# Kernel tuning notes

Measured on AMD Instinct MI355X. Metric: run time of the kernel, lower is better.

The kernel has to match this reference:

```python
import jax, jax.numpy as jnp
import numpy as np

B, S, H, D = 2, 2048, 16, 64


def setup_inputs() -> dict:
    key0 = jax.random.key(0)
    kq, kk = jax.random.split(key0)
    query = jax.random.normal(kq, (B, S, H, D), dtype=jnp.float32)
    key = jax.random.normal(kk, (B, S, H, D), dtype=jnp.float32)
    # causal mask, broadcastable to [B, H, q, k]
    mask = jnp.tril(jnp.ones((S, S), dtype=bool))[None, None, :, :]
    mask = jnp.broadcast_to(mask, (B, 1, S, S))
    return {"query": query, "key": key, "mask": mask}


def reference(query, key, mask):
    dtype = query.dtype
    qk_features = query.shape[-1]
    q = query / jnp.sqrt(qk_features).astype(dtype)
    # [B, H, q, k]
    attn_weights = jnp.einsum('...qhd,...khd->...hqk', q, key)
    big_neg = jnp.finfo(dtype).min
    attn_weights = jnp.where(mask, attn_weights, big_neg)
    attn_weights = jax.nn.softmax(attn_weights).astype(dtype)
    return attn_weights
```

## Files before the change

kernel.cpp:

```cpp
#include <hip/hip_runtime.h>
#include <stdint.h>
#include <stddef.h>

#define B_ 2
#define H_ 16
#define S_ 2048
#define D_ 64

#define TQ 32
#define TK 256
#define NW 4
#define BLK (NW*64)
#define NQT (S_/TQ)
#define NBLK_F (B_*H_*NQT)
#define NBLK_S (32*36)
#define NBLK_W (32*8*4)

typedef __attribute__((ext_vector_type(8))) short bf16x8;
typedef __attribute__((ext_vector_type(4))) float f32x4;

__device__ __forceinline__ unsigned short f2bf(float f) {
  union { float f; uint32_t u; } v; v.f = f;
  uint32_t r = v.u + 0x7FFFu + ((v.u >> 16) & 1u);
  return (unsigned short)(r >> 16);
}

__device__ __forceinline__ void stage_k(const f32x4* kp, unsigned short* ldsK,
                                        int b, int h, int kc, int tid) {
#pragma unroll
  for (int i = 0; i < 8; ++i) {
    const int g  = i * BLK + tid;
    const int kl = g >> 3;
    const int gd = g & 7;
    const size_t gb = (((size_t)b * S_ + (kc * TK + kl)) * H_ + h) * (D_ / 4) + gd * 2;
    f32x4 v0 = kp[gb];
    f32x4 v1 = kp[gb + 1];
    bf16x8 bv;
    bv[0] = (short)f2bf(v0.x); bv[1] = (short)f2bf(v0.y);
    bv[2] = (short)f2bf(v0.z); bv[3] = (short)f2bf(v0.w);
    bv[4] = (short)f2bf(v1.x); bv[5] = (short)f2bf(v1.y);
    bv[6] = (short)f2bf(v1.z); bv[7] = (short)f2bf(v1.w);
    const int idx = (kl * D_ + gd * 8) ^ ((kl & 7) << 3);
    *reinterpret_cast<bf16x8*>(&ldsK[idx]) = bv;
  }
}

__device__ __forceinline__ void stage_q(const f32x4* qp, unsigned short (*ldsQ)[72],
                                        int b, int h, int qb, int tid) {
#pragma unroll
  for (int i = 0; i < 2; ++i) {
    const int g   = i * BLK + tid;
    const int row = g >> 4;
    const int d4  = g & 15;
    f32x4 v = qp[(((size_t)b * S_ + (qb + row)) * H_ + h) * (D_ / 4) + d4];
    unsigned short* dst = &ldsQ[row][d4 * 4];
    dst[0] = f2bf(v.x * 0.125f);
    dst[1] = f2bf(v.y * 0.125f);
    dst[2] = f2bf(v.z * 0.125f);
    dst[3] = f2bf(v.w * 0.125f);
  }
}

__device__ __forceinline__ void mfma_tile(const unsigned short* ldsK,
                                          const bf16x8 qfr[2][2],
                                          f32x4 acc[4][2], int w, int colk, int rg) {
#pragma unroll
  for (int kf = 0; kf < 4; ++kf) {
    const int krow = w * 64 + kf * 16 + colk;
    const int i0 = (krow * D_ + rg * 8) ^ ((krow & 7) << 3);
    const int i1 = (krow * D_ + 32 + rg * 8) ^ ((krow & 7) << 3);
    bf16x8 a0 = *reinterpret_cast<const bf16x8*>(&ldsK[i0]);
    bf16x8 a1 = *reinterpret_cast<const bf16x8*>(&ldsK[i1]);
#pragma unroll
    for (int qf = 0; qf < 2; ++qf) {
      acc[kf][qf] = __builtin_amdgcn_mfma_f32_16x16x32_bf16(a0, qfr[qf][0], acc[kf][qf], 0, 0, 0);
      acc[kf][qf] = __builtin_amdgcn_mfma_f32_16x16x32_bf16(a1, qfr[qf][1], acc[kf][qf], 0, 0, 0);
    }
  }
}

__device__ __forceinline__ void load_qfr(const unsigned short (*ldsQ)[72],
                                         bf16x8 qfr[2][2], int colk, int rg) {
#pragma unroll
  for (int qf = 0; qf < 2; ++qf)
#pragma unroll
    for (int hh = 0; hh < 2; ++hh)
      qfr[qf][hh] = *reinterpret_cast<const bf16x8*>(&ldsQ[qf * 16 + colk][hh * 32 + rg * 8]);
}

__global__ __launch_bounds__(BLK, 4)
void attn_sums_v4(const float* __restrict__ Qg, const float* __restrict__ Kg,
                  float* __restrict__ wsPart) {
  __shared__ unsigned short ldsK[TK * D_];
  __shared__ unsigned short ldsQ[TQ][72];
  __shared__ float ldsSum[NW][2][16];

  const int tid  = threadIdx.x;
  const int lane = tid & 63;
  const int w    = tid >> 6;
  const int colk = lane & 15;
  const int rg   = lane >> 4;

  int bid = (int)blockIdx.x;
  bid = (bid & 7) * (NBLK_S / 8) + (bid >> 3);
  const int bh = bid / 36;
  int j = bid - bh * 36;
  int kc = 0, base = 0;
  while (j >= base + (8 - kc)) { base += 8 - kc; ++kc; }
  const int ci = j - base;
  const int qt0 = kc * 8 + ci * 8;
  const int b = bh >> 4, h = bh & (H_ - 1);

  const f32x4* qp = reinterpret_cast<const f32x4*>(Qg);
  const f32x4* kp = reinterpret_cast<const f32x4*>(Kg);

  stage_k(kp, ldsK, b, h, kc, tid);

  for (int i = 0; i < 8; ++i) {
    const int qt = qt0 + i;
    const int qb = qt * TQ;
    __syncthreads();
    stage_q(qp, ldsQ, b, h, qb, tid);
    __syncthreads();
    bf16x8 qfr[2][2];
    load_qfr(ldsQ, qfr, colk, rg);
    f32x4 acc[4][2];
#pragma unroll
    for (int kf = 0; kf < 4; ++kf)
#pragma unroll
      for (int qf = 0; qf < 2; ++qf) acc[kf][qf] = (f32x4)0.0f;
    mfma_tile(ldsK, qfr, acc, w, colk, rg);

    float rsum[2] = {0.f, 0.f};
#pragma unroll
    for (int kf = 0; kf < 4; ++kf)
#pragma unroll
      for (int qf = 0; qf < 2; ++qf)
#pragma unroll
        for (int r = 0; r < 4; ++r) {
          const int kk = kc * TK + w * 64 + kf * 16 + rg * 4 + r;
          const int qq = qb + qf * 16 + colk;
          rsum[qf] += (kk <= qq) ? __expf(acc[kf][qf][r]) : 0.f;
        }
#pragma unroll
    for (int qf = 0; qf < 2; ++qf) {
      float v = rsum[qf];
      v += __shfl_xor(v, 16);
      v += __shfl_xor(v, 32);
      rsum[qf] = v;
    }
    if (rg == 0) { ldsSum[w][0][colk] = rsum[0]; ldsSum[w][1][colk] = rsum[1]; }
    __syncthreads();
    if (tid < 32) {
      const int qf = tid >> 4, ck = tid & 15;
      const float s = ldsSum[0][qf][ck] + ldsSum[1][qf][ck] +
                      ldsSum[2][qf][ck] + ldsSum[3][qf][ck];
      wsPart[((size_t)bh * 8 + kc) * S_ + qb + tid] = s;
    }
  }
}

__global__ __launch_bounds__(BLK, 4)
void attn_store_v4(const float* __restrict__ Qg, const float* __restrict__ Kg,
                   const float* __restrict__ wsPart, float* __restrict__ Og) {
  __shared__ unsigned short ldsK[TK * D_];
  __shared__ unsigned short ldsQ[TQ][72];
  __shared__ float rinvL[512];

  const int tid  = threadIdx.x;
  const int lane = tid & 63;
  const int w    = tid >> 6;
  const int colk = lane & 15;
  const int rg   = lane >> 4;

  int bid = (int)blockIdx.x;
  bid = (bid & 7) * (NBLK_W / 8) + (bid >> 3);
  const int bh = bid >> 5;
  const int r5 = bid & 31;
  const int kc = r5 >> 2;
  const int qg = r5 & 3;
  const int b = bh >> 4, h = bh & (H_ - 1);
  const int kmin = kc * TK;
  const int row0 = qg * 512;

  if (kmin > row0 + 511) {
    const int rr = tid >> 3, cg = tid & 7;
    f32x4 z = {0.f, 0.f, 0.f, 0.f};
#pragma unroll
    for (int tr = 0; tr < 16; ++tr) {
      float* rp = Og + ((size_t)bh * S_ + row0 + tr * 32 + rr) * S_ + kmin;
#pragma unroll
      for (int c = 0; c < 8; ++c)
        __builtin_nontemporal_store(z, reinterpret_cast<f32x4*>(rp + (c * 8 + cg) * 4));
    }
    return;
  }

  const f32x4* qp = reinterpret_cast<const f32x4*>(Qg);
  const f32x4* kp = reinterpret_cast<const f32x4*>(Kg);

  stage_k(kp, ldsK, b, h, kc, tid);

  for (int lr = tid; lr < 512; lr += BLK) {
    const int q = row0 + lr;
    if (q >= kmin) {
      float s = 0.f;
      const int top = q >> 8;
      for (int c2 = 0; c2 <= top; ++c2)
        s += wsPart[((size_t)bh * 8 + c2) * S_ + q];
      rinvL[lr] = 1.0f / s;
    }
  }

  bool synced = false;
  for (int i = 0; i < 16; ++i) {
    const int qt = qg * 16 + i;
    const int qb = qt * TQ;
    float* outT = Og + ((size_t)bh * S_ + qb) * S_ + kmin;

    if (kmin > qb + 31) {
      const int rr = tid >> 3, cg = tid & 7;
      f32x4 z = {0.f, 0.f, 0.f, 0.f};
      float* rp = outT + (size_t)rr * S_;
#pragma unroll
      for (int c = 0; c < 8; ++c)
        __builtin_nontemporal_store(z, reinterpret_cast<f32x4*>(rp + (c * 8 + cg) * 4));
      continue;
    }

    __syncthreads();
    (void)synced;
    stage_q(qp, ldsQ, b, h, qb, tid);
    __syncthreads();
    bf16x8 qfr[2][2];
    load_qfr(ldsQ, qfr, colk, rg);
    f32x4 acc[4][2];
#pragma unroll
    for (int kf = 0; kf < 4; ++kf)
#pragma unroll
      for (int qf = 0; qf < 2; ++qf) acc[kf][qf] = (f32x4)0.0f;
    mfma_tile(ldsK, qfr, acc, w, colk, rg);

#pragma unroll
    for (int kf = 0; kf < 4; ++kf)
#pragma unroll
      for (int qf = 0; qf < 2; ++qf) {
        const int qq = qb + qf * 16 + colk;
        const float ri = rinvL[i * 32 + qf * 16 + colk];
        f32x4 o;
#pragma unroll
        for (int r = 0; r < 4; ++r) {
          const int kk = kmin + w * 64 + kf * 16 + rg * 4 + r;
          o[r] = (kk <= qq) ? __expf(acc[kf][qf][r]) * ri : 0.f;
        }
        __builtin_nontemporal_store(o, reinterpret_cast<f32x4*>(
            outT + (size_t)(qf * 16 + colk) * S_ + w * 64 + kf * 16 + rg * 4));
      }
  }
}

__global__ __launch_bounds__(BLK, 4)
void attn_weights_fused(const float* __restrict__ Qg, const float* __restrict__ Kg,
                        float* __restrict__ Og) {
  __shared__ unsigned short ldsK[TK * D_];
  __shared__ unsigned short ldsQ[TQ][72];
  __shared__ float ldsSum[NW][2][16];

  const int tid  = threadIdx.x;
  const int lane = tid & 63;
  const int w    = tid >> 6;
  const int colk = lane & 15;
  const int rg   = lane >> 4;

  int bid = (int)blockIdx.x;
  bid = (bid & 7) * (NBLK_F / 8) + (bid >> 3);
  const int qt = bid & (NQT - 1);
  const int bh = bid >> 6;
  const int h  = bh & (H_ - 1);
  const int b  = bh >> 4;
  const int qb = qt * TQ;
  const int tmax = qb >> 8;

  float* outp = Og + ((size_t)bh * S_ + qb) * S_;
  {
    const int row = tid >> 3;
    f32x4 z = {0.f, 0.f, 0.f, 0.f};
    float* rp = outp + (size_t)row * S_;
    for (int c = (tmax + 1) * (TK / 4) + (tid & 7); c < S_ / 4; c += 8)
      *reinterpret_cast<f32x4*>(rp + c * 4) = z;
  }
  const f32x4* qp = reinterpret_cast<const f32x4*>(Qg);
  const f32x4* kp = reinterpret_cast<const f32x4*>(Kg);
  stage_q(qp, ldsQ, b, h, qb, tid);
  __syncthreads();
  bf16x8 qfr[2][2];
  load_qfr(ldsQ, qfr, colk, rg);
  float rsum[2] = {0.f, 0.f};
  for (int t = 0; t <= tmax; ++t) {
    stage_k(kp, ldsK, b, h, t, tid);
    __syncthreads();
    f32x4 acc[4][2];
#pragma unroll
    for (int kf = 0; kf < 4; ++kf)
#pragma unroll
      for (int qf = 0; qf < 2; ++qf) acc[kf][qf] = (f32x4)0.0f;
    mfma_tile(ldsK, qfr, acc, w, colk, rg);
#pragma unroll
    for (int kf = 0; kf < 4; ++kf)
#pragma unroll
      for (int qf = 0; qf < 2; ++qf)
#pragma unroll
        for (int r = 0; r < 4; ++r) {
          const int kk = t * TK + w * 64 + kf * 16 + rg * 4 + r;
          const int qq = qb + qf * 16 + colk;
          rsum[qf] += (kk <= qq) ? __expf(acc[kf][qf][r]) : 0.f;
        }
    __syncthreads();
  }
#pragma unroll
  for (int qf = 0; qf < 2; ++qf) {
    float v = rsum[qf];
    v += __shfl_xor(v, 16);
    v += __shfl_xor(v, 32);
    rsum[qf] = v;
  }
  if (rg == 0) { ldsSum[w][0][colk] = rsum[0]; ldsSum[w][1][colk] = rsum[1]; }
  __syncthreads();
  float rinv[2];
#pragma unroll
  for (int qf = 0; qf < 2; ++qf)
    rinv[qf] = 1.0f / (ldsSum[0][qf][colk] + ldsSum[1][qf][colk] +
                       ldsSum[2][qf][colk] + ldsSum[3][qf][colk]);
  for (int t = 0; t <= tmax; ++t) {
    stage_k(kp, ldsK, b, h, t, tid);
    __syncthreads();
    f32x4 acc[4][2];
#pragma unroll
    for (int kf = 0; kf < 4; ++kf)
#pragma unroll
      for (int qf = 0; qf < 2; ++qf) acc[kf][qf] = (f32x4)0.0f;
    mfma_tile(ldsK, qfr, acc, w, colk, rg);
#pragma unroll
    for (int kf = 0; kf < 4; ++kf)
#pragma unroll
      for (int qf = 0; qf < 2; ++qf) {
        f32x4 o;
#pragma unroll
        for (int r = 0; r < 4; ++r) {
          const int kk = t * TK + w * 64 + kf * 16 + rg * 4 + r;
          const int qq = qb + qf * 16 + colk;
          o[r] = (kk <= qq) ? __expf(acc[kf][qf][r]) * rinv[qf] : 0.f;
        }
        *reinterpret_cast<f32x4*>(outp + (size_t)(qf * 16 + colk) * S_ +
                                  t * TK + w * 64 + kf * 16 + rg * 4) = o;
      }
    __syncthreads();
  }
}

extern "C" void kernel_launch(void* const* d_in, const int* in_sizes, int n_in,
                              void* d_out, int out_size, void* d_ws, size_t ws_size,
                              hipStream_t stream) {
  const float* Qg = (const float*)d_in[0];
  const float* Kg = (const float*)d_in[1];
  float* Og = (float*)d_out;
  const size_t need = (size_t)32 * 8 * S_ * sizeof(float);
  if (ws_size >= need) {
    float* wsPart = (float*)d_ws;
    attn_sums_v4 <<<dim3(NBLK_S), dim3(BLK), 0, stream>>>(Qg, Kg, wsPart);
    attn_store_v4<<<dim3(NBLK_W), dim3(BLK), 0, stream>>>(Qg, Kg, wsPart, Og);
  } else {
    attn_weights_fused<<<dim3(NBLK_F), dim3(BLK), 0, stream>>>(Qg, Kg, Og);
  }
}
```

Before: 161.6 us.

## Fuse sum and store passes into one cooperative kernel with grid sync

Result: slower. 420.7 us (+160.3%).

```diff
diff --git a/kernel.cpp b/kernel.cpp
--- a/kernel.cpp
+++ b/kernel.cpp
@@ -1,4 +1,5 @@
 #include <hip/hip_runtime.h>
+#include <hip/hip_cooperative_groups.h>
 #include <stdint.h>
 #include <stddef.h>
 
@@ -15,6 +16,7 @@
 #define NBLK_F (B_*H_*NQT)
 #define NBLK_S (32*36)
 #define NBLK_W (32*8*4)
+#define NBLK_C (32*8*4)
 
 typedef __attribute__((ext_vector_type(8))) short bf16x8;
 typedef __attribute__((ext_vector_type(4))) float f32x4;
@@ -45,6 +47,155 @@
   }
 }
 
+__device__ __forceinline__ void load_qfr_g(const float* __restrict__ Qg,
+                                           int b, int h, int qb,
+                                           int colk, int rg, bf16x8 qfr[2][2]) {
+#pragma unroll
+  for (int qf = 0; qf < 2; ++qf) {
+    const float* rowp = Qg + (((size_t)b * S_ + qb + qf * 16 + colk) * H_ + h) * D_;
+#pragma unroll
+    for (int hh = 0; hh < 2; ++hh) {
+      const float* p = rowp + hh * 32 + rg * 8;
+      f32x4 v0 = *reinterpret_cast<const f32x4*>(p);
+      f32x4 v1 = *reinterpret_cast<const f32x4*>(p + 4);
+      bf16x8 q8;
+      q8[0] = (short)f2bf(v0.x * 0.125f); q8[1] = (short)f2bf(v0.y * 0.125f);
+      q8[2] = (short)f2bf(v0.z * 0.125f); q8[3] = (short)f2bf(v0.w * 0.125f);
+      q8[4] = (short)f2bf(v1.x * 0.125f); q8[5] = (short)f2bf(v1.y * 0.125f);
+      q8[6] = (short)f2bf(v1.z * 0.125f); q8[7] = (short)f2bf(v1.w * 0.125f);
+      qfr[qf][hh] = q8;
+    }
+  }
+}
+
+__global__ __launch_bounds__(BLK, 4)
+void attn_coop(const float* __restrict__ Qg, const float* __restrict__ Kg,
+               float* __restrict__ wsPart, float* __restrict__ Og) {
+  __shared__ unsigned short ldsK[TK * D_];
+
+  const int tid  = threadIdx.x;
+  const int lane = tid & 63;
+  const int w    = tid >> 6;
+  const int colk = lane & 15;
+  const int rg   = lane >> 4;
+
+  const int bid = (int)blockIdx.x;
+  const int bh = bid >> 5;
+  const int r5 = bid & 31;
+  const int kc = r5 >> 2;
+  const int qg = r5 & 3;
+  const int b = bh >> 4, h = bh & (H_ - 1);
+  const int kmin = kc * TK;
+  const int row0 = qg * 512;
+
+  cooperative_groups::grid_group grid = cooperative_groups::this_grid();
+
+  if (kmin > row0 + 511) {
+    f32x4 z = {0.f, 0.f, 0.f, 0.f};
+#pragma unroll 4
+    for (int it = 0; it < 128; ++it) {
+      const int g = it * BLK + tid;
+      const int row = row0 + (g >> 6);
+      const int cg = g & 63;
+      __builtin_nontemporal_store(z, reinterpret_cast<f32x4*>(
+          Og + ((size_t)bh * S_ + row) * S_ + kmin + cg * 4));
+    }
+    grid.sync();
+    return;
+  }
+
+  const f32x4* kp = reinterpret_cast<const f32x4*>(Kg);
+  stage_k(kp, ldsK, b, h, kc, tid);
+  __syncthreads();
+
+  for (int i = w; i < 16; i += NW) {
+    const int qb = row0 + i * 32;
+    if (qb + 31 < kmin) {
+      f32x4 z = {0.f, 0.f, 0.f, 0.f};
+      float* tp = Og + ((size_t)bh * S_ + qb) * S_ + kmin;
+#pragma unroll 4
+      for (int it = 0; it < 32; ++it)
+        __builtin_nontemporal_store(z, reinterpret_cast<f32x4*>(tp + (size_t)it * S_ + lane * 4));
+      continue;
+    }
+    bf16x8 qfr[2][2];
+    load_qfr_g(Qg, b, h, qb, colk, rg, qfr);
+    float rs[2] = {0.f, 0.f};
+#pragma unroll
+    for (int kf = 0; kf < 16; ++kf) {
+      const int krow = kf * 16 + colk;
+      const int i0 = (krow * D_ + rg * 8) ^ ((krow & 7) << 3);
+      const int i1 = (krow * D_ + 32 + rg * 8) ^ ((krow & 7) << 3);
+      bf16x8 a0 = *reinterpret_cast<const bf16x8*>(&ldsK[i0]);
+      bf16x8 a1 = *reinterpret_cast<const bf16x8*>(&ldsK[i1]);
+#pragma unroll
+      for (int qf = 0; qf < 2; ++qf) {
+        f32x4 acc = (f32x4)0.0f;
+        acc = __builtin_amdgcn_mfma_f32_16x16x32_bf16(a0, qfr[qf][0], acc, 0, 0, 0);
+        acc = __builtin_amdgcn_mfma_f32_16x16x32_bf16(a1, qfr[qf][1], acc, 0, 0, 0);
+        const int qq = qb + qf * 16 + colk;
+#pragma unroll
+        for (int r = 0; r < 4; ++r) {
+          const int kk = kmin + kf * 16 + rg * 4 + r;
+          rs[qf] += (kk <= qq) ? __expf(acc[r]) : 0.f;
+        }
+      }
+    }
+#pragma unroll
+    for (int qf = 0; qf < 2; ++qf) {
+      float v = rs[qf];
+      v += __shfl_xor(v, 16);
+      v += __shfl_xor(v, 32);
+      if (rg == 0)
+        wsPart[((size_t)bh * 8 + kc) * S_ + qb + qf * 16 + colk] = v;
+    }
+  }
+
+  __threadfence();
+  grid.sync();
+
+  for (int i = w; i < 16; i += NW) {
+    const int qb = row0 + i * 32;
+    if (qb + 31 < kmin) continue;
+    float rinv[2];
+#pragma unroll
+    for (int qf = 0; qf < 2; ++qf) {
+      const int q = qb + qf * 16 + colk;
+      float s = 0.f;
+      const int top = q >> 8;
+      for (int c2 = 0; c2 <= top; ++c2)
+        s += wsPart[((size_t)bh * 8 + c2) * S_ + q];
+      rinv[qf] = 1.0f / s;
+    }
+    bf16x8 qfr[2][2];
+    load_qfr_g(Qg, b, h, qb, colk, rg, qfr);
+    float* tp = Og + ((size_t)bh * S_ + qb) * S_ + kmin;
+#pragma unroll
+    for (int kf = 0; kf < 16; ++kf) {
+      const int krow = kf * 16 + colk;
+      const int i0 = (krow * D_ + rg * 8) ^ ((krow & 7) << 3);
+      const int i1 = (krow * D_ + 32 + rg * 8) ^ ((krow & 7) << 3);
+      bf16x8 a0 = *reinterpret_cast<const bf16x8*>(&ldsK[i0]);
+      bf16x8 a1 = *reinterpret_cast<const bf16x8*>(&ldsK[i1]);
+#pragma unroll
+      for (int qf = 0; qf < 2; ++qf) {
+        f32x4 acc = (f32x4)0.0f;
+        acc = __builtin_amdgcn_mfma_f32_16x16x32_bf16(a0, qfr[qf][0], acc, 0, 0, 0);
+        acc = __builtin_amdgcn_mfma_f32_16x16x32_bf16(a1, qfr[qf][1], acc, 0, 0, 0);
+        const int qq = qb + qf * 16 + colk;
+        f32x4 o;
+#pragma unroll
+        for (int r = 0; r < 4; ++r) {
+          const int kk = kmin + kf * 16 + rg * 4 + r;
+          o[r] = (kk <= qq) ? __expf(acc[r]) * rinv[qf] : 0.f;
+        }
+        __builtin_nontemporal_store(o, reinterpret_cast<f32x4*>(
+            tp + (size_t)(qf * 16 + colk) * S_ + kf * 16 + rg * 4));
+      }
+    }
+  }
+}
+
 __device__ __forceinline__ void stage_q(const f32x4* qp, unsigned short (*ldsQ)[72],
                                         int b, int h, int qb, int tid) {
 #pragma unroll
@@ -212,7 +363,6 @@
     }
   }
 
-  bool synced = false;
   for (int i = 0; i < 16; ++i) {
     const int qt = qg * 16 + i;
     const int qb = qt * TQ;
@@ -229,7 +379,6 @@
     }
 
     __syncthreads();
-    (void)synced;
     stage_q(qp, ldsQ, b, h, qb, tid);
     __syncthreads();
     bf16x8 qfr[2][2];
@@ -367,8 +516,15 @@
   const size_t need = (size_t)32 * 8 * S_ * sizeof(float);
   if (ws_size >= need) {
     float* wsPart = (float*)d_ws;
-    attn_sums_v4 <<<dim3(NBLK_S), dim3(BLK), 0, stream>>>(Qg, Kg, wsPart);
-    attn_store_v4<<<dim3(NBLK_W), dim3(BLK), 0, stream>>>(Qg, Kg, wsPart, Og);
+    void* args[] = {(void*)&Qg, (void*)&Kg, (void*)&wsPart, (void*)&Og};
+    hipError_t e = hipLaunchCooperativeKernel(
+        reinterpret_cast<void*>(attn_coop), dim3(NBLK_C), dim3(BLK),
+        args, 0, stream);
+    if (e != hipSuccess) {
+      (void)hipGetLastError();
+      attn_sums_v4 <<<dim3(NBLK_S), dim3(BLK), 0, stream>>>(Qg, Kg, wsPart);
+      attn_store_v4<<<dim3(NBLK_W), dim3(BLK), 0, stream>>>(Qg, Kg, wsPart, Og);
+    }
   } else {
     attn_weights_fused<<<dim3(NBLK_F), dim3(BLK), 0, stream>>>(Qg, Kg, Og);
   }
```

## Give each wave its own query tile in store kernel, drop per-tile block syncs

Applied to the files above, without the earlier changes.

Measured after the change: 179.9 us. +11.3%, slower.

```diff
diff --git a/kernel.cpp b/kernel.cpp
--- a/kernel.cpp
+++ b/kernel.cpp
@@ -61,6 +61,27 @@
   }
 }
 
+__device__ __forceinline__ void load_qfr_g(const float* __restrict__ Qg,
+                                           int b, int h, int qb,
+                                           int colk, int rg, bf16x8 qfr[2][2]) {
+#pragma unroll
+  for (int qf = 0; qf < 2; ++qf) {
+    const float* rowp = Qg + (((size_t)b * S_ + qb + qf * 16 + colk) * H_ + h) * D_;
+#pragma unroll
+    for (int hh = 0; hh < 2; ++hh) {
+      const float* p = rowp + hh * 32 + rg * 8;
+      f32x4 v0 = *reinterpret_cast<const f32x4*>(p);
+      f32x4 v1 = *reinterpret_cast<const f32x4*>(p + 4);
+      bf16x8 q8;
+      q8[0] = (short)f2bf(v0.x * 0.125f); q8[1] = (short)f2bf(v0.y * 0.125f);
+      q8[2] = (short)f2bf(v0.z * 0.125f); q8[3] = (short)f2bf(v0.w * 0.125f);
+      q8[4] = (short)f2bf(v1.x * 0.125f); q8[5] = (short)f2bf(v1.y * 0.125f);
+      q8[6] = (short)f2bf(v1.z * 0.125f); q8[7] = (short)f2bf(v1.w * 0.125f);
+      qfr[qf][hh] = q8;
+    }
+  }
+}
+
 __device__ __forceinline__ void mfma_tile(const unsigned short* ldsK,
                                           const bf16x8 qfr[2][2],
                                           f32x4 acc[4][2], int w, int colk, int rg) {
@@ -161,10 +182,9 @@
 }
 
 __global__ __launch_bounds__(BLK, 4)
-void attn_store_v4(const float* __restrict__ Qg, const float* __restrict__ Kg,
+void attn_store_v5(const float* __restrict__ Qg, const float* __restrict__ Kg,
                    const float* __restrict__ wsPart, float* __restrict__ Og) {
   __shared__ unsigned short ldsK[TK * D_];
-  __shared__ unsigned short ldsQ[TQ][72];
   __shared__ float rinvL[512];
 
   const int tid  = threadIdx.x;
@@ -184,21 +204,19 @@
   const int row0 = qg * 512;
 
   if (kmin > row0 + 511) {
-    const int rr = tid >> 3, cg = tid & 7;
     f32x4 z = {0.f, 0.f, 0.f, 0.f};
-#pragma unroll
-    for (int tr = 0; tr < 16; ++tr) {
-      float* rp = Og + ((size_t)bh * S_ + row0 + tr * 32 + rr) * S_ + kmin;
-#pragma unroll
-      for (int c = 0; c < 8; ++c)
-        __builtin_nontemporal_store(z, reinterpret_cast<f32x4*>(rp + (c * 8 + cg) * 4));
+#pragma unroll 4
+    for (int it = 0; it < 128; ++it) {
+      const int g = it * BLK + tid;
+      const int row = row0 + (g >> 6);
+      const int cg = g & 63;
+      __builtin_nontemporal_store(z, reinterpret_cast<f32x4*>(
+          Og + ((size_t)bh * S_ + row) * S_ + kmin + cg * 4));
     }
     return;
   }
 
-  const f32x4* qp = reinterpret_cast<const f32x4*>(Qg);
   const f32x4* kp = reinterpret_cast<const f32x4*>(Kg);
-
   stage_k(kp, ldsK, b, h, kc, tid);
 
   for (int lr = tid; lr < 512; lr += BLK) {
@@ -211,51 +229,50 @@
       rinvL[lr] = 1.0f / s;
     }
   }
-
-  bool synced = false;
-  for (int i = 0; i < 16; ++i) {
-    const int qt = qg * 16 + i;
-    const int qb = qt * TQ;
-    float* outT = Og + ((size_t)bh * S_ + qb) * S_ + kmin;
-
-    if (kmin > qb + 31) {
-      const int rr = tid >> 3, cg = tid & 7;
+  __syncthreads();
+
+  for (int i = w; i < 16; i += NW) {
+    const int qb = row0 + i * 32;
+    float* tp = Og + ((size_t)bh * S_ + qb) * S_ + kmin;
+
+    if (qb + 31 < kmin) {
       f32x4 z = {0.f, 0.f, 0.f, 0.f};
-      float* rp = outT + (size_t)rr * S_;
-#pragma unroll
-      for (int c = 0; c < 8; ++c)
-        __builtin_nontemporal_store(z, reinterpret_cast<f32x4*>(rp + (c * 8 + cg) * 4));
+#pragma unroll 4
+      for (int it = 0; it < 32; ++it)
+        __builtin_nontemporal_store(z, reinterpret_cast<f32x4*>(
+            tp + (size_t)it * S_ + lane * 4));
       continue;
     }
 
-    __syncthreads();
-    (void)synced;
-    stage_q(qp, ldsQ, b, h, qb, tid);
-    __syncthreads();
     bf16x8 qfr[2][2];
-    load_qfr(ldsQ, qfr, colk, rg);
-    f32x4 acc[4][2];
-#pragma unroll
-    for (int kf = 0; kf < 4; ++kf)
-#pragma unroll
-      for (int qf = 0; qf < 2; ++qf) acc[kf][qf] = (f32x4)0.0f;
-    mfma_tile(ldsK, qfr, acc, w, colk, rg);
-
-#pragma unroll
-    for (int kf = 0; kf < 4; ++kf)
+    load_qfr_g(Qg, b, h, qb, colk, rg, qfr);
+    const float rinv0 = rinvL[i * 32 + colk];
+    const float rinv1 = rinvL[i * 32 + 16 + colk];
+
+#pragma unroll
+    for (int kf = 0; kf < 16; ++kf) {
+      const int krow = kf * 16 + colk;
+      const int i0 = (krow * D_ + rg * 8) ^ ((krow & 7) << 3);
+      const int i1 = (krow * D_ + 32 + rg * 8) ^ ((krow & 7) << 3);
+      bf16x8 a0 = *reinterpret_cast<const bf16x8*>(&ldsK[i0]);
+      bf16x8 a1 = *reinterpret_cast<const bf16x8*>(&ldsK[i1]);
 #pragma unroll
       for (int qf = 0; qf < 2; ++qf) {
+        f32x4 acc = (f32x4)0.0f;
+        acc = __builtin_amdgcn_mfma_f32_16x16x32_bf16(a0, qfr[qf][0], acc, 0, 0, 0);
+        acc = __builtin_amdgcn_mfma_f32_16x16x32_bf16(a1, qfr[qf][1], acc, 0, 0, 0);
         const int qq = qb + qf * 16 + colk;
-        const float ri = rinvL[i * 32 + qf * 16 + colk];
+        const float ri = qf ? rinv1 : rinv0;
         f32x4 o;
 #pragma unroll
         for (int r = 0; r < 4; ++r) {
-          const int kk = kmin + w * 64 + kf * 16 + rg * 4 + r;
-          o[r] = (kk <= qq) ? __expf(acc[kf][qf][r]) * ri : 0.f;
+          const int kk = kmin + kf * 16 + rg * 4 + r;
+          o[r] = (kk <= qq) ? __expf(acc[r]) * ri : 0.f;
         }
         __builtin_nontemporal_store(o, reinterpret_cast<f32x4*>(
-            outT + (size_t)(qf * 16 + colk) * S_ + w * 64 + kf * 16 + rg * 4));
+            tp + (size_t)(qf * 16 + colk) * S_ + kf * 16 + rg * 4));
       }
+    }
   }
 }
 
@@ -368,7 +385,7 @@
   if (ws_size >= need) {
     float* wsPart = (float*)d_ws;
     attn_sums_v4 <<<dim3(NBLK_S), dim3(BLK), 0, stream>>>(Qg, Kg, wsPart);
-    attn_store_v4<<<dim3(NBLK_W), dim3(BLK), 0, stream>>>(Qg, Kg, wsPart, Og);
+    attn_store_v5<<<dim3(NBLK_W), dim3(BLK), 0, stream>>>(Qg, Kg, wsPart, Og);
   } else {
     attn_weights_fused<<<dim3(NBLK_F), dim3(BLK), 0, stream>>>(Qg, Kg, Og);
   }
```

## Merge sums and store kernels into one ticket-scheduled persistent launch

Applied to the files above, without the earlier changes.

New measurement: 215.7 us. 1.33x slower.

```diff
diff --git a/kernel.cpp b/kernel.cpp
--- a/kernel.cpp
+++ b/kernel.cpp
@@ -13,8 +13,11 @@
 #define BLK (NW*64)
 #define NQT (S_/TQ)
 #define NBLK_F (B_*H_*NQT)
-#define NBLK_S (32*36)
-#define NBLK_W (32*8*4)
+
+#define NZ  384
+#define NS  1152
+#define NWC 640
+#define NTOT (NZ+NS+NWC)
 
 typedef __attribute__((ext_vector_type(8))) short bf16x8;
 typedef __attribute__((ext_vector_type(4))) float f32x4;
@@ -61,6 +64,15 @@
   }
 }
 
+__device__ __forceinline__ void load_qfr(const unsigned short (*ldsQ)[72],
+                                         bf16x8 qfr[2][2], int colk, int rg) {
+#pragma unroll
+  for (int qf = 0; qf < 2; ++qf)
+#pragma unroll
+    for (int hh = 0; hh < 2; ++hh)
+      qfr[qf][hh] = *reinterpret_cast<const bf16x8*>(&ldsQ[qf * 16 + colk][hh * 32 + rg * 8]);
+}
+
 __device__ __forceinline__ void mfma_tile(const unsigned short* ldsK,
                                           const bf16x8 qfr[2][2],
                                           f32x4 acc[4][2], int w, int colk, int rg) {
@@ -79,21 +91,18 @@
   }
 }
 
-__device__ __forceinline__ void load_qfr(const unsigned short (*ldsQ)[72],
-                                         bf16x8 qfr[2][2], int colk, int rg) {
-#pragma unroll
-  for (int qf = 0; qf < 2; ++qf)
-#pragma unroll
-    for (int hh = 0; hh < 2; ++hh)
-      qfr[qf][hh] = *reinterpret_cast<const bf16x8*>(&ldsQ[qf * 16 + colk][hh * 32 + rg * 8]);
-}
-
 __global__ __launch_bounds__(BLK, 4)
-void attn_sums_v4(const float* __restrict__ Qg, const float* __restrict__ Kg,
-                  float* __restrict__ wsPart) {
-  __shared__ unsigned short ldsK[TK * D_];
-  __shared__ unsigned short ldsQ[TQ][72];
-  __shared__ float ldsSum[NW][2][16];
+void attn_merged(const float* __restrict__ Qg, const float* __restrict__ Kg,
+                 int* __restrict__ ctrl, float* __restrict__ wsPart,
+                 float* __restrict__ Og) {
+  __shared__ alignas(16) unsigned char smem[39424];
+  unsigned short* ldsK = reinterpret_cast<unsigned short*>(smem);
+  unsigned short (*ldsQ)[72] = reinterpret_cast<unsigned short (*)[72]>(smem + 32768);
+  float* ldsTail = reinterpret_cast<float*>(smem + 37376);
+  __shared__ int tktS;
+
+  int* cnt    = ctrl;
+  int* ticket = ctrl + 256;
 
   const int tid  = threadIdx.x;
   const int lane = tid & 63;
@@ -101,161 +110,174 @@
   const int colk = lane & 15;
   const int rg   = lane >> 4;
 
-  int bid = (int)blockIdx.x;
-  bid = (bid & 7) * (NBLK_S / 8) + (bid >> 3);
-  const int bh = bid / 36;
-  int j = bid - bh * 36;
-  int kc = 0, base = 0;
-  while (j >= base + (8 - kc)) { base += 8 - kc; ++kc; }
-  const int ci = j - base;
-  const int qt0 = kc * 8 + ci * 8;
-  const int b = bh >> 4, h = bh & (H_ - 1);
+  if (tid == 0)
+    tktS = __hip_atomic_fetch_add(ticket, 1, __ATOMIC_RELAXED, __HIP_MEMORY_SCOPE_AGENT);
+  __syncthreads();
+  const int t = tktS;
 
   const f32x4* qp = reinterpret_cast<const f32x4*>(Qg);
   const f32x4* kp = reinterpret_cast<const f32x4*>(Kg);
 
-  stage_k(kp, ldsK, b, h, kc, tid);
-
-  for (int i = 0; i < 8; ++i) {
-    const int qt = qt0 + i;
-    const int qb = qt * TQ;
-    __syncthreads();
-    stage_q(qp, ldsQ, b, h, qb, tid);
-    __syncthreads();
-    bf16x8 qfr[2][2];
-    load_qfr(ldsQ, qfr, colk, rg);
-    f32x4 acc[4][2];
-#pragma unroll
-    for (int kf = 0; kf < 4; ++kf)
-#pragma unroll
-      for (int qf = 0; qf < 2; ++qf) acc[kf][qf] = (f32x4)0.0f;
-    mfma_tile(ldsK, qfr, acc, w, colk, rg);
-
-    float rsum[2] = {0.f, 0.f};
-#pragma unroll
-    for (int kf = 0; kf < 4; ++kf)
-#pragma unroll
-      for (int qf = 0; qf < 2; ++qf)
-#pragma unroll
-        for (int r = 0; r < 4; ++r) {
-          const int kk = kc * TK + w * 64 + kf * 16 + rg * 4 + r;
+  if (t < NZ + NS && (t & 3) == 3) {
+    const int z  = t >> 2;
+    const int bh = z / 12;
+    const int p  = z % 12;
+    const int qg = (p < 6) ? 0 : (p < 10) ? 1 : 2;
+    const int kc = (qg == 0) ? 2 + p : (qg == 1) ? p - 2 : p - 4;
+    const int row0 = qg * 512, kmin = kc * TK;
+    f32x4 zf = {0.f, 0.f, 0.f, 0.f};
+#pragma unroll 4
+    for (int it = 0; it < 128; ++it) {
+      const int g = it * BLK + tid;
+      const int row = row0 + (g >> 6);
+      const int cg = g & 63;
+      __builtin_nontemporal_store(zf, reinterpret_cast<f32x4*>(
+          Og + ((size_t)bh * S_ + row) * S_ + kmin + cg * 4));
+    }
+    return;
+  }
+
+  if (t < NZ + NS) {
+    const int si = (t >> 2) * 3 + (t & 3);
+    const int bh = si / 36;
+    int j = si % 36;
+    int kc = 0, base = 0;
+    while (j >= base + (8 - kc)) { base += 8 - kc; ++kc; }
+    const int ci = j - base;
+    const int qt0 = kc * 8 + ci * 8;
+    const int b = bh >> 4, h = bh & (H_ - 1);
+
+    stage_k(kp, ldsK, b, h, kc, tid);
+
+    for (int i = 0; i < 8; ++i) {
+      const int qb = (qt0 + i) * TQ;
+      __syncthreads();
+      stage_q(qp, ldsQ, b, h, qb, tid);
+      __syncthreads();
+      bf16x8 qfr[2][2];
+      load_qfr(ldsQ, qfr, colk, rg);
+      f32x4 acc[4][2];
+#pragma unroll
+      for (int kf = 0; kf < 4; ++kf)
+#pragma unroll
+        for (int qf = 0; qf < 2; ++qf) acc[kf][qf] = (f32x4)0.0f;
+      mfma_tile(ldsK, qfr, acc, w, colk, rg);
+
+      float rsum[2] = {0.f, 0.f};
+#pragma unroll
+      for (int kf = 0; kf < 4; ++kf)
+#pragma unroll
+        for (int qf = 0; qf < 2; ++qf)
+#pragma unroll
+          for (int r = 0; r < 4; ++r) {
+            const int kk = kc * TK + w * 64 + kf * 16 + rg * 4 + r;
+            const int qq = qb + qf * 16 + colk;
+            rsum[qf] += (kk <= qq) ? __expf(acc[kf][qf][r]) : 0.f;
+          }
+#pragma unroll
+      for (int qf = 0; qf < 2; ++qf) {
+        float v = rsum[qf];
+        v += __shfl_xor(v, 16);
+        v += __shfl_xor(v, 32);
+        rsum[qf] = v;
+      }
+      if (rg == 0) {
+        ldsTail[w * 32 + colk]      = rsum[0];
+        ldsTail[w * 32 + 16 + colk] = rsum[1];
+      }
+      __syncthreads();
+      if (tid < 32) {
+        const int qf = tid >> 4, ck = tid & 15;
+        const float s = ldsTail[0 * 32 + qf * 16 + ck] + ldsTail[1 * 32 + qf * 16 + ck] +
+                        ldsTail[2 * 32 + qf * 16 + ck] + ldsTail[3 * 32 + qf * 16 + ck];
+        wsPart[((size_t)bh * 8 + kc) * S_ + qb + tid] = s;
+      }
+    }
+    __syncthreads();
+    if (tid == 0)
+      __hip_atomic_fetch_add(&cnt[bh * 8 + kc + ci], 1,
+                             __ATOMIC_RELEASE, __HIP_MEMORY_SCOPE_AGENT);
+    return;
+  }
+
+  {
+    static const int QGt[20] = {0,1,1,1,2,2,2,2,2,3,3,3,3,3,3,3, 0,1,2,3};
+    static const int KCt[20] = {0,0,1,2,0,1,2,3,4,0,1,2,3,4,5,6, 1,3,5,7};
+    const int wi = t - (NZ + NS);
+    const int bh = wi & 31;
+    const int pr = wi >> 5;
+    const int qg = QGt[pr], kc = KCt[pr];
+    const int b = bh >> 4, h = bh & (H_ - 1);
+    const int kmin = kc * TK;
+    const int row0 = qg * 512;
+    float* rinvL = ldsTail;
+
+    stage_k(kp, ldsK, b, h, kc, tid);
+
+    if (tid == 0) {
+      const int s0 = 2 * qg;
+      while (__hip_atomic_load(&cnt[bh * 8 + s0], __ATOMIC_ACQUIRE,
+                               __HIP_MEMORY_SCOPE_AGENT) <= s0)
+        __builtin_amdgcn_s_sleep(32);
+      while (__hip_atomic_load(&cnt[bh * 8 + s0 + 1], __ATOMIC_ACQUIRE,
+                               __HIP_MEMORY_SCOPE_AGENT) <= s0 + 1)
+        __builtin_amdgcn_s_sleep(32);
+    }
+    __syncthreads();
+
+    for (int lr = tid; lr < 512; lr += BLK) {
+      const int q = row0 + lr;
+      if (q >= kmin) {
+        float s = 0.f;
+        const int top = q >> 8;
+        for (int c2 = 0; c2 <= top; ++c2)
+          s += wsPart[((size_t)bh * 8 + c2) * S_ + q];
+        rinvL[lr] = 1.0f / s;
+      }
+    }
+
+    for (int i = 0; i < 16; ++i) {
+      const int qb = row0 + i * TQ;
+      float* outT = Og + ((size_t)bh * S_ + qb) * S_ + kmin;
+
+      if (kmin > qb + 31) {
+        const int rr = tid >> 3, cg = tid & 7;
+        f32x4 z = {0.f, 0.f, 0.f, 0.f};
+        float* rp = outT + (size_t)rr * S_;
+#pragma unroll
+        for (int c = 0; c < 8; ++c)
+          __builtin_nontemporal_store(z, reinterpret_cast<f32x4*>(rp + (c * 8 + cg) * 4));
+        continue;
+      }
+
+      __syncthreads();
+      stage_q(qp, ldsQ, b, h, qb, tid);
+      __syncthreads();
+      bf16x8 qfr[2][2];
+      load_qfr(ldsQ, qfr, colk, rg);
+      f32x4 acc[4][2];
+#pragma unroll
+      for (int kf = 0; kf < 4; ++kf)
+#pragma unroll
+        for (int qf = 0; qf < 2; ++qf) acc[kf][qf] = (f32x4)0.0f;
+      mfma_tile(ldsK, qfr, acc, w, colk, rg);
+
+#pragma unroll
+      for (int kf = 0; kf < 4; ++kf)
+#pragma unroll
+        for (int qf = 0; qf < 2; ++qf) {
           const int qq = qb + qf * 16 + colk;
-          rsum[qf] += (kk <= qq) ? __expf(acc[kf][qf][r]) : 0.f;
+          const float ri = rinvL[i * 32 + qf * 16 + colk];
+          f32x4 o;
+#pragma unroll
+          for (int r = 0; r < 4; ++r) {
+            const int kk = kmin + w * 64 + kf * 16 + rg * 4 + r;
+            o[r] = (kk <= qq) ? __expf(acc[kf][qf][r]) * ri : 0.f;
+          }
+          __builtin_nontemporal_store(o, reinterpret_cast<f32x4*>(
+              outT + (size_t)(qf * 16 + colk) * S_ + w * 64 + kf * 16 + rg * 4));
         }
-#pragma unroll
-    for (int qf = 0; qf < 2; ++qf) {
-      float v = rsum[qf];
-      v += __shfl_xor(v, 16);
-      v += __shfl_xor(v, 32);
-      rsum[qf] = v;
-    }
-    if (rg == 0) { ldsSum[w][0][colk] = rsum[0]; ldsSum[w][1][colk] = rsum[1]; }
-    __syncthreads();
-    if (tid < 32) {
-      const int qf = tid >> 4, ck = tid & 15;
-      const float s = ldsSum[0][qf][ck] + ldsSum[1][qf][ck] +
-                      ldsSum[2][qf][ck] + ldsSum[3][qf][ck];
-      wsPart[((size_t)bh * 8 + kc) * S_ + qb + tid] = s;
-    }
-  }
-}
-
-__global__ __launch_bounds__(BLK, 4)
-void attn_store_v4(const float* __restrict__ Qg, const float* __restrict__ Kg,
-                   const float* __restrict__ wsPart, float* __restrict__ Og) {
-  __shared__ unsigned short ldsK[TK * D_];
-  __shared__ unsigned short ldsQ[TQ][72];
-  __shared__ float rinvL[512];
-
-  const int tid  = threadIdx.x;
-  const int lane = tid & 63;
-  const int w    = tid >> 6;
-  const int colk = lane & 15;
-  const int rg   = lane >> 4;
-
-  int bid = (int)blockIdx.x;
-  bid = (bid & 7) * (NBLK_W / 8) + (bid >> 3);
-  const int bh = bid >> 5;
-  const int r5 = bid & 31;
-  const int kc = r5 >> 2;
-  const int qg = r5 & 3;
-  const int b = bh >> 4, h = bh & (H_ - 1);
-  const int kmin = kc * TK;
-  const int row0 = qg * 512;
-
-  if (kmin > row0 + 511) {
-    const int rr = tid >> 3, cg = tid & 7;
-    f32x4 z = {0.f, 0.f, 0.f, 0.f};
-#pragma unroll
-    for (int tr = 0; tr < 16; ++tr) {
-      float* rp = Og + ((size_t)bh * S_ + row0 + tr * 32 + rr) * S_ + kmin;
-#pragma unroll
-      for (int c = 0; c < 8; ++c)
-        __builtin_nontemporal_store(z, reinterpret_cast<f32x4*>(rp + (c * 8 + cg) * 4));
-    }
-    return;
-  }
-
-  const f32x4* qp = reinterpret_cast<const f32x4*>(Qg);
-  const f32x4* kp = reinterpret_cast<const f32x4*>(Kg);
-
-  stage_k(kp, ldsK, b, h, kc, tid);
-
-  for (int lr = tid; lr < 512; lr += BLK) {
-    const int q = row0 + lr;
-    if (q >= kmin) {
-      float s = 0.f;
-      const int top = q >> 8;
-      for (int c2 = 0; c2 <= top; ++c2)
-        s += wsPart[((size_t)bh * 8 + c2) * S_ + q];
-      rinvL[lr] = 1.0f / s;
-    }
-  }
-
-  bool synced = false;
-  for (int i = 0; i < 16; ++i) {
-    const int qt = qg * 16 + i;
-    const int qb = qt * TQ;
-    float* outT = Og + ((size_t)bh * S_ + qb) * S_ + kmin;
-
-    if (kmin > qb + 31) {
-      const int rr = tid >> 3, cg = tid & 7;
-      f32x4 z = {0.f, 0.f, 0.f, 0.f};
-      float* rp = outT + (size_t)rr * S_;
-#pragma unroll
-      for (int c = 0; c < 8; ++c)
-        __builtin_nontemporal_store(z, reinterpret_cast<f32x4*>(rp + (c * 8 + cg) * 4));
-      continue;
-    }
-
-    __syncthreads();
-    (void)synced;
-    stage_q(qp, ldsQ, b, h, qb, tid);
-    __syncthreads();
-    bf16x8 qfr[2][2];
-    load_qfr(ldsQ, qfr, colk, rg);
-    f32x4 acc[4][2];
-#pragma unroll
-    for (int kf = 0; kf < 4; ++kf)
-#pragma unroll
-      for (int qf = 0; qf < 2; ++qf) acc[kf][qf] = (f32x4)0.0f;
-    mfma_tile(ldsK, qfr, acc, w, colk, rg);
-
-#pragma unroll
-    for (int kf = 0; kf < 4; ++kf)
-#pragma unroll
-      for (int qf = 0; qf < 2; ++qf) {
-        const int qq = qb + qf * 16 + colk;
-        const float ri = rinvL[i * 32 + qf * 16 + colk];
-        f32x4 o;
-#pragma unroll
-        for (int r = 0; r < 4; ++r) {
-          const int kk = kmin + w * 64 + kf * 16 + rg * 4 + r;
-          o[r] = (kk <= qq) ? __expf(acc[kf][qf][r]) * ri : 0.f;
-        }
-        __builtin_nontemporal_store(o, reinterpret_cast<f32x4*>(
-            outT + (size_t)(qf * 16 + colk) * S_ + w * 64 + kf * 16 + rg * 4));
-      }
+    }
   }
 }
 
@@ -364,11 +386,12 @@
   const float* Qg = (const float*)d_in[0];
   const float* Kg = (const float*)d_in[1];
   float* Og = (float*)d_out;
-  const size_t need = (size_t)32 * 8 * S_ * sizeof(float);
+  const size_t need = 4096 + (size_t)32 * 8 * S_ * sizeof(float);
   if (ws_size >= need) {
-    float* wsPart = (float*)d_ws;
-    attn_sums_v4 <<<dim3(NBLK_S), dim3(BLK), 0, stream>>>(Qg, Kg, wsPart);
-    attn_store_v4<<<dim3(NBLK_W), dim3(BLK), 0, stream>>>(Qg, Kg, wsPart, Og);
+    int* ctrl = (int*)d_ws;
+    float* wsPart = (float*)((char*)d_ws + 4096);
+    hipMemsetAsync(d_ws, 0, 4096, stream);
+    attn_merged<<<dim3(NTOT), dim3(BLK), 0, stream>>>(Qg, Kg, ctrl, wsPart, Og);
   } else {
     attn_weights_fused<<<dim3(NBLK_F), dim3(BLK), 0, stream>>>(Qg, Kg, Og);
   }
```
